# Kernel optimization log

Hardware: AMD Instinct MI355X
Metric: run time of the kernel (lower is better)

Reference implementation:

```python
import jax, jax.numpy as jnp
import numpy as np

B, T = 128, 64
N_IN, H1, H2, N_OUT = 2048, 2048, 1024, 128
BETA = 0.95
THRESH = 1.0  # snn.Leaky default threshold


def spike(x):
    # Heaviside firing function (forward of snntorch ATan surrogate)
    return (x > 0).astype(x.dtype)


def setup_inputs() -> dict:
    key = jax.random.key(0)
    ks = jax.random.split(key, 5)

    def linear_params(k, fan_in, fan_out):
        k1, k2 = jax.random.split(k)
        bound = 1.0 / np.sqrt(fan_in)  # torch nn.Linear default init
        W = jax.random.uniform(k1, (fan_out, fan_in), minval=-bound, maxval=bound, dtype=jnp.float32)
        b = jax.random.uniform(k2, (fan_out,), minval=-bound, maxval=bound, dtype=jnp.float32)
        return W, b

    W0, b0 = linear_params(ks[0], N_IN, N_IN)
    W1, b1 = linear_params(ks[1], N_IN, H1)
    W2, b2 = linear_params(ks[2], H1, H2)
    W3, b3 = linear_params(ks[3], H2, N_OUT)
    x = jax.random.normal(ks[4], (B, T, N_IN), dtype=jnp.float32)
    return {"x": x, "W0": W0, "b0": b0, "W1": W1, "b1": b1,
            "W2": W2, "b2": b2, "W3": W3, "b3": b3}


def _lif(cur, mem):
    # snntorch Leaky (reset_mechanism='subtract'): reset computed from incoming mem
    reset = spike(mem - THRESH)
    mem_new = BETA * mem + cur - reset * THRESH
    spk = spike(mem_new - THRESH)
    return spk, mem_new


def reference(x, W0, b0, W1, b1, W2, b2, W3, b3):
    Bb = x.shape[0]
    dt = x.dtype
    mems0 = (jnp.zeros((Bb, N_IN), dt), jnp.zeros((Bb, H1), dt),
             jnp.zeros((Bb, H2), dt), jnp.zeros((Bb, N_OUT), dt))
    x_tbf = jnp.swapaxes(x, 0, 1)  # [T, B, N_IN]

    def step(carry, x_t):
        m0, m1, m2, m3 = carry
        s0, m0 = _lif(x_t @ W0.T + b0, m0)
        s1, m1 = _lif(s0 @ W1.T + b1, m1)
        s2, m2 = _lif(s1 @ W2.T + b2, m2)
        s3, m3 = _lif(s2 @ W3.T + b3, m3)
        return (m0, m1, m2, m3), (s3, m3)

    _, (spk3, mem3) = jax.lax.scan(step, mems0, x_tbf)
    # [T, B, N_OUT] -> [B, T, N_OUT]
    return jnp.swapaxes(spk3, 0, 1), jnp.swapaxes(mem3, 0, 1)
```

## Files before the change

kernel.cpp:

```cpp
#include <hip/hip_runtime.h>
#include <cstddef>
#include <cstdint>


#define BETA 0.95f

static constexpr int B_ = 128;
static constexpr int T_ = 64;
static constexpr int M_ = B_ * T_;
static constexpr int NOUT = 128;

typedef __bf16 bf16x8 __attribute__((ext_vector_type(8)));
typedef _Float16 f16x8 __attribute__((ext_vector_type(8)));
typedef float f32x4 __attribute__((ext_vector_type(4)));
typedef ushort u16x8 __attribute__((ext_vector_type(8)));

__device__ __forceinline__ ushort f32_bf16_rne(float f) {
  uint32_t u = __float_as_uint(f);
  uint32_t r = u + 0x7FFFu + ((u >> 16) & 1u);
  return (ushort)(r >> 16);
}
__device__ __forceinline__ float bf16_f32(ushort h) {
  return __uint_as_float(((uint32_t)h) << 16);
}
__device__ __forceinline__ ushort h2u(_Float16 h) {
  union { _Float16 h; ushort u; } v; v.h = h; return v.u;
}
__device__ __forceinline__ _Float16 u2h(ushort u) {
  union { ushort u; _Float16 h; } v; v.u = u; return v.h;
}

__global__ __launch_bounds__(256) void split2_f16(
    const float* __restrict__ S, ushort* __restrict__ oh,
    ushort* __restrict__ ol, int K, int nslots)
{
  int g = blockIdx.x * 256 + threadIdx.x;
  if (g >= nslots) return;
  int spr = K >> 3;
  int row = g / spr;
  int sl = g - row * spr;
  int kb = sl >> 3;
  int slot = sl & 7;
  int pslot = (slot & 4) | ((slot & 3) ^ ((row >> 1) & 3));
  const float* src = S + (size_t)row * K + (kb << 6) + (slot << 3);
  size_t dst = (size_t)row * K + (kb << 6) + (pslot << 3);
  u16x8 vh, vl;
#pragma unroll
  for (int i = 0; i < 8; ++i) {
    float f = src[i];
    _Float16 h = (_Float16)f;
    float hf = (float)h;
    if (fabsf(hf) < 6.103515625e-05f) { h = (_Float16)0.0f; hf = 0.0f; }
    float l = (f - hf) * 4096.0f;
    _Float16 hl = (_Float16)l;
    vh[i] = h2u(h);
    vl[i] = h2u(hl);
  }
  *reinterpret_cast<u16x8*>(oh + dst) = vh;
  *reinterpret_cast<u16x8*>(ol + dst) = vl;
}

__global__ __launch_bounds__(256) void split3_swz(
    const float* __restrict__ S, ushort* __restrict__ o1,
    ushort* __restrict__ o2, ushort* __restrict__ o3,
    int K, int nslots)
{
  int g = blockIdx.x * 256 + threadIdx.x;
  if (g >= nslots) return;
  int spr = K >> 3;
  int row = g / spr;
  int sl = g - row * spr;
  int kb = sl >> 3;
  int slot = sl & 7;
  int pslot = slot ^ (row & 7);
  const float* src = S + (size_t)row * K + (kb << 6) + (slot << 3);
  size_t dst = (size_t)row * K + (kb << 6) + (pslot << 3);
  u16x8 v1, v2, v3;
#pragma unroll
  for (int i = 0; i < 8; ++i) {
    float f = src[i];
    ushort h1 = f32_bf16_rne(f);
    float r = f - bf16_f32(h1);
    ushort h2 = f32_bf16_rne(r);
    float r2 = r - bf16_f32(h2);
    ushort h3 = f32_bf16_rne(r2);
    v1[i] = h1; v2[i] = h2; v3[i] = h3;
  }
  *reinterpret_cast<u16x8*>(o1 + dst) = v1;
  *reinterpret_cast<u16x8*>(o2 + dst) = v2;
  *reinterpret_cast<u16x8*>(o3 + dst) = v3;
}

__global__ __launch_bounds__(256) void gemm_seg(
    const ushort* __restrict__ A0, const ushort* __restrict__ A1,
    const ushort* __restrict__ A2,
    const ushort* __restrict__ B0, const ushort* __restrict__ B1,
    const ushort* __restrict__ B2,
    int P, int apack, int bpack, int K, int N, int accum,
    float* __restrict__ C)
{
  __shared__ ushort As[128 * 64];
  __shared__ ushort Bs[128 * 64];

  const int tid = threadIdx.x;
  const int lane = tid & 63;
  const int wid = tid >> 6;
  const int wr = wid >> 1, wc = wid & 1;
  const int lane15 = lane & 15;
  const int lhi = lane >> 4;
  const int rswz = lane15 & 7;
  const int lrow = lane >> 3, lslot = lane & 7;

  int nwg = gridDim.x * gridDim.y;
  int bid = blockIdx.y * gridDim.x + blockIdx.x;
  int cpx = nwg >> 3;
  int sw = (bid & 7) * cpx + (bid >> 3);
  int bx = sw % gridDim.x, by = sw / gridDim.x;
  const int bm = by * 128, bn = bx * 128;

  f32x4 acc[4][4];
#pragma unroll
  for (int i = 0; i < 4; ++i)
#pragma unroll
    for (int j = 0; j < 4; ++j)
      acc[i][j] = (f32x4){0.f, 0.f, 0.f, 0.f};

  const bool isA = (wid < 2);
  ushort* lbase = isA ? As : Bs;
  const int rowbase0 = isA ? bm : bn;
  const int chunk0 = (wid & 1) * 8;

  for (int p = 0; p < P; ++p) {
    int ai = (apack >> (2 * p)) & 3;
    int bi = (bpack >> (2 * p)) & 3;
    const ushort* Ap = ai == 0 ? A0 : (ai == 1 ? A1 : A2);
    const ushort* Bp = bi == 0 ? B0 : (bi == 1 ? B1 : B2);
    const ushort* gsrc = isA ? Ap : Bp;
    for (int k0 = 0; k0 < K; k0 += 64) {
      __syncthreads();
#pragma unroll
      for (int c = 0; c < 8; ++c) {
        int chunk = chunk0 + c;
        int row = chunk * 8 + lrow;
        const ushort* g = gsrc + (size_t)(rowbase0 + row) * K + k0 + (lslot << 3);
        __builtin_amdgcn_global_load_lds(
            (const __attribute__((address_space(1))) void*)(g),
            (__attribute__((address_space(3))) void*)(lbase + chunk * 512),
            16, 0, 0);
      }
      __syncthreads();
#pragma unroll
      for (int kk = 0; kk < 2; ++kk) {
        int sp = ((kk << 2) | lhi) ^ rswz;
        bf16x8 af[4], bg[4];
#pragma unroll
        for (int i = 0; i < 4; ++i)
          af[i] = *(const bf16x8*)(As + (wr * 64 + i * 16 + lane15) * 64 + sp * 8);
#pragma unroll
        for (int j = 0; j < 4; ++j)
          bg[j] = *(const bf16x8*)(Bs + (wc * 64 + j * 16 + lane15) * 64 + sp * 8);
#pragma unroll
        for (int i = 0; i < 4; ++i)
#pragma unroll
          for (int j = 0; j < 4; ++j)
            acc[i][j] = __builtin_amdgcn_mfma_f32_16x16x32_bf16(
                af[i], bg[j], acc[i][j], 0, 0, 0);
      }
    }
  }

#pragma unroll
  for (int j = 0; j < 4; ++j) {
    int col = bn + wc * 64 + j * 16 + lane15;
#pragma unroll
    for (int i = 0; i < 4; ++i) {
      f32x4 v = acc[i][j];
      int r0 = bm + wr * 64 + i * 16 + lhi * 4;
      if (accum) {
#pragma unroll
        for (int r = 0; r < 4; ++r) {
          size_t idx = (size_t)(r0 + r) * N + col;
          C[idx] = C[idx] + v[r];
        }
      } else {
#pragma unroll
        for (int r = 0; r < 4; ++r)
          C[(size_t)(r0 + r) * N + col] = v[r];
      }
    }
  }
}

template<int NB, int MODE>
__global__ __launch_bounds__(512) void gemm2(
    const ushort* __restrict__ A,
    const ushort* __restrict__ Bs0, const ushort* __restrict__ Bs1,
    int NT, int K, int N,
    float* __restrict__ curM, ushort* __restrict__ curC)
{
  __shared__ __align__(16) ushort lds[32768 + 2 * 2 * NB * 4096];

  const int tid = threadIdx.x;
  const int lane = tid & 63;
  const int wid = tid >> 6;
  const int wm = wid >> 1;
  const int wn = wid & 1;
  const int lane15 = lane & 15;
  const int lhi = lane >> 4;
  const int sg2 = lhi ^ ((lane15 >> 1) & 3);

  int nwg = gridDim.x * gridDim.y;
  int bid = blockIdx.y * gridDim.x + blockIdx.x;
  int cpx = nwg >> 3;
  int sw = (bid & 7) * cpx + (bid >> 3);
  int bx = sw % gridDim.x, by = sw / gridDim.x;
  const int bm = by * 256, bn = bx * 128;

  const int sr2 = tid >> 2;
  const int sg = tid & 3;

  auto stage = [&](int t1, int h, int d) {
    const int k0 = t1 * 64 + h * 32;
#pragma unroll
    for (int l = 0; l < 2; ++l) {
      int row = sr2 + l * 128;
      __builtin_amdgcn_global_load_lds(
          (const __attribute__((address_space(1))) void*)(A + (size_t)(bm + row) * K + k0 + sg * 8),
          (__attribute__((address_space(3))) void*)(lds + d * 16384 + h * 8192 + row * 32 + sg * 8),
          16, 0, 0);
    }
#pragma unroll
    for (int s = 0; s < NB; ++s) {
      const ushort* Bp = (s == 0) ? Bs0 : Bs1;
      __builtin_amdgcn_global_load_lds(
          (const __attribute__((address_space(1))) void*)(Bp + (size_t)(bn + sr2) * K + k0 + sg * 8),
          (__attribute__((address_space(3))) void*)(lds + 32768 + ((d * 2 + h) * NB + s) * 4096 + sr2 * 32 + sg * 8),
          16, 0, 0);
    }
  };

  f32x4 accM[4][4], accC[4][4];
#pragma unroll
  for (int i = 0; i < 4; ++i)
#pragma unroll
    for (int j = 0; j < 4; ++j) {
      accM[i][j] = (f32x4){0.f, 0.f, 0.f, 0.f};
      accC[i][j] = (f32x4){0.f, 0.f, 0.f, 0.f};
    }

  stage(0, 0, 0);
  stage(0, 1, 0);
  if constexpr (NB == 2) asm volatile("s_waitcnt vmcnt(4)" ::: "memory");
  if constexpr (NB == 1) asm volatile("s_waitcnt vmcnt(3)" ::: "memory");
  asm volatile("s_barrier" ::: "memory");

  for (int t = 0; t < NT; ++t) {
    const int d = t & 1;
#pragma unroll
    for (int h = 0; h < 2; ++h) {
      f16x8 af[4];
      const ushort* Ab = lds + (d * 2 + h) * 8192;
#pragma unroll
      for (int i = 0; i < 4; ++i)
        af[i] = *(const f16x8*)(Ab + (wm * 64 + i * 16 + lane15) * 32 + sg2 * 8);

      if (t < NT - 1) {
        stage(t + 1, h, d ^ 1);
        if constexpr (NB == 2) asm volatile("s_waitcnt vmcnt(4)" ::: "memory");
        if constexpr (NB == 1) asm volatile("s_waitcnt vmcnt(3)" ::: "memory");
      } else if (h == 0) {
        asm volatile("s_waitcnt vmcnt(0)" ::: "memory");
      }
      asm volatile("s_barrier" ::: "memory");

      __builtin_amdgcn_s_setprio(1);
#pragma unroll
      for (int s = 0; s < NB; ++s) {
        const ushort* Bb = lds + 32768 + ((d * 2 + h) * NB + s) * 4096;
        f16x8 bf[4];
#pragma unroll
        for (int j = 0; j < 4; ++j)
          bf[j] = *(const f16x8*)(Bb + (wn * 64 + j * 16 + lane15) * 32 + sg2 * 8);
        if (MODE == 0 && s == 0) {
#pragma unroll
          for (int i = 0; i < 4; ++i)
#pragma unroll
            for (int j = 0; j < 4; ++j)
              accM[i][j] = __builtin_amdgcn_mfma_f32_16x16x32_f16(af[i], bf[j], accM[i][j], 0, 0, 0);
        } else {
#pragma unroll
          for (int i = 0; i < 4; ++i)
#pragma unroll
            for (int j = 0; j < 4; ++j)
              accC[i][j] = __builtin_amdgcn_mfma_f32_16x16x32_f16(af[i], bf[j], accC[i][j], 0, 0, 0);
        }
      }
      __builtin_amdgcn_s_setprio(0);
      asm volatile("s_barrier" ::: "memory");
    }
  }

#pragma unroll
  for (int i = 0; i < 4; ++i) {
    int r0 = bm + wm * 64 + i * 16 + lhi * 4;
#pragma unroll
    for (int j = 0; j < 4; ++j) {
      int col = bn + wn * 64 + j * 16 + lane15;
      f32x4 vc = accC[i][j];
      if (MODE == 0) {
        f32x4 vm = accM[i][j];
#pragma unroll
        for (int r = 0; r < 4; ++r) {
          size_t idx = (size_t)(r0 + r) * N + col;
          curM[idx] = vm[r];
          curC[idx] = h2u((_Float16)vc[r]);
        }
      } else {
#pragma unroll
        for (int r = 0; r < 4; ++r) {
          size_t idx = (size_t)(r0 + r) * N + col;
          float old = (float)u2h(curC[idx]);
          curC[idx] = h2u((_Float16)(old + vc[r]));
        }
      }
    }
  }
}

__global__ __launch_bounds__(256) void lif_comb(
    const float* __restrict__ curM, const ushort* __restrict__ curC,
    const float* __restrict__ bias, ushort* __restrict__ spk,
    int N, int total, int fmt)
{
  int g = blockIdx.x * 256 + threadIdx.x;
  if (g >= total) return;
  int b = g / N, n = g - b * N;
  int nb = n >> 6;
  int slot = (n >> 3) & 7;
  int nlow = n & 7;
  float bv = bias[n];
  const ushort one = fmt ? (ushort)0x3C00 : (ushort)0x3F80;
  float mem = 0.f;
  for (int t = 0; t < T_; ++t) {
    int m = b * T_ + t;
    size_t idx = (size_t)m * N + n;
    float mm = __fmaf_rn((float)u2h(curC[idx]), 2.44140625e-4f, curM[idx]);
    float c = __fadd_rn(mm, bv);
    float reset = ((mem - 1.0f) > 0.0f) ? 1.0f : 0.0f;
    mem = __fmul_rn(BETA, mem);
    mem = __fadd_rn(mem, c);
    mem = __fadd_rn(mem, -reset);
    ushort sv = ((mem - 1.0f) > 0.0f) ? one : (ushort)0;
    int ps = fmt ? ((slot & 4) | ((slot & 3) ^ ((m >> 1) & 3)))
                 : (slot ^ (m & 7));
    spk[(size_t)m * N + (nb << 6) + (ps << 3) + nlow] = sv;
  }
}

__global__ __launch_bounds__(256) void lif_final(
    const float* __restrict__ cur_in, const float* __restrict__ bias,
    float* __restrict__ spk_out, float* __restrict__ mem_out, int N, int total)
{
  int g = blockIdx.x * 256 + threadIdx.x;
  if (g >= total) return;
  int b = g / N, n = g - b * N;
  size_t base = (size_t)b * T_ * N + n;
  float bv = bias[n];
  float mem = 0.f;
  for (int t = 0; t < T_; ++t) {
    size_t idx = base + (size_t)t * N;
    float c = __fadd_rn(cur_in[idx], bv);
    float reset = ((mem - 1.0f) > 0.0f) ? 1.0f : 0.0f;
    mem = __fmul_rn(BETA, mem);
    mem = __fadd_rn(mem, c);
    mem = __fadd_rn(mem, -reset);
    spk_out[idx] = ((mem - 1.0f) > 0.0f) ? 1.0f : 0.0f;
    mem_out[idx] = mem;
  }
}

extern "C" void kernel_launch(void* const* d_in, const int* in_sizes, int n_in,
                              void* d_out, int out_size, void* d_ws, size_t ws_size,
                              hipStream_t stream)
{
  const float* x  = (const float*)d_in[0];
  const float* W0 = (const float*)d_in[1];
  const float* b0 = (const float*)d_in[2];
  const float* W1 = (const float*)d_in[3];
  const float* b1 = (const float*)d_in[4];
  const float* W2 = (const float*)d_in[5];
  const float* b2 = (const float*)d_in[6];
  const float* W3 = (const float*)d_in[7];
  const float* b3 = (const float*)d_in[8];
  float* out = (float*)d_out;

  char* ws = (char*)d_ws;
  size_t off = 0;
  auto take = [&](size_t bytes) -> char* {
    char* p = ws + off;
    off += (bytes + 255) & ~(size_t)255;
    return p;
  };

  ushort* w0h = (ushort*)take((size_t)2048 * 2048 * 2);
  ushort* w0l = (ushort*)take((size_t)2048 * 2048 * 2);
  ushort* w1h = (ushort*)take((size_t)2048 * 2048 * 2);
  ushort* w1l = (ushort*)take((size_t)2048 * 2048 * 2);
  ushort* w2h = (ushort*)take((size_t)1024 * 2048 * 2);
  ushort* w2l = (ushort*)take((size_t)1024 * 2048 * 2);
  ushort* w3s[3];
  for (int i = 0; i < 3; ++i) w3s[i] = (ushort*)take((size_t)128 * 1024 * 2);
  ushort* xh = (ushort*)take((size_t)M_ * 2048 * 2);
  ushort* xl = (ushort*)take((size_t)M_ * 2048 * 2);
  ushort* s0 = (ushort*)take((size_t)M_ * 2048 * 2);
  float* curM = (float*)take((size_t)M_ * 2048 * 4);
  ushort* curC = (ushort*)take((size_t)M_ * 2048 * 2);
  ushort* s1 = xh;
  ushort* s2 = xl;

  dim3 blk(256);
  dim3 fblk(512);

  {
    int ns = 2048 * 2048 / 8;
    split2_f16<<<(ns + 255) / 256, blk, 0, stream>>>(W0, w0h, w0l, 2048, ns);
    split2_f16<<<(ns + 255) / 256, blk, 0, stream>>>(W1, w1h, w1l, 2048, ns);
    ns = 1024 * 2048 / 8;
    split2_f16<<<(ns + 255) / 256, blk, 0, stream>>>(W2, w2h, w2l, 2048, ns);
    ns = 128 * 1024 / 8;
    split3_swz<<<(ns + 255) / 256, blk, 0, stream>>>(W3, w3s[0], w3s[1], w3s[2], 1024, ns);
    ns = M_ * 2048 / 8;
    split2_f16<<<(ns + 255) / 256, blk, 0, stream>>>(x, xh, xl, 2048, ns);
  }

  {
    dim3 grid(2048 / 128, M_ / 256);
    gemm2<2, 0><<<grid, fblk, 0, stream>>>(xh, w0h, w0l, 32, 2048, 2048, curM, curC);
    gemm2<1, 1><<<grid, fblk, 0, stream>>>(xl, w0h, w0h, 32, 2048, 2048, curM, curC);
    lif_comb<<<(B_ * 2048) / 256, blk, 0, stream>>>(curM, curC, b0, s0, 2048, B_ * 2048, 1);
  }
  {
    dim3 grid(2048 / 128, M_ / 256);
    gemm2<2, 0><<<grid, fblk, 0, stream>>>(s0, w1h, w1l, 32, 2048, 2048, curM, curC);
    lif_comb<<<(B_ * 2048) / 256, blk, 0, stream>>>(curM, curC, b1, s1, 2048, B_ * 2048, 1);
  }
  {
    dim3 grid(1024 / 128, M_ / 256);
    gemm2<2, 0><<<grid, fblk, 0, stream>>>(s1, w2h, w2l, 32, 2048, 1024, curM, curC);
    lif_comb<<<(B_ * 1024) / 256, blk, 0, stream>>>(curM, curC, b2, s2, 1024, B_ * 1024, 0);
  }
  {
    dim3 grid(128 / 128, M_ / 128);
    gemm_seg<<<grid, blk, 0, stream>>>(s2, s2, s2, w3s[0], w3s[1], w3s[2],
                                       1, 0, 0, 1024, 128, 0, curM);
    gemm_seg<<<grid, blk, 0, stream>>>(s2, s2, s2, w3s[0], w3s[1], w3s[2],
                                       2, 0, 1 | (2 << 2), 1024, 128, 1, curM);
    float* spk3 = out;
    float* mem3 = out + (size_t)M_ * NOUT;
    lif_final<<<(B_ * NOUT) / 256, blk, 0, stream>>>(curM, b3, spk3, mem3, NOUT, B_ * NOUT);
  }
}
```

Measured before the change: 591.6 us.

## Fuse LIF recurrence into GEMM epilogues and drop fp32 current buffer

```diff
diff --git a/kernel.cpp b/kernel.cpp
--- a/kernel.cpp
+++ b/kernel.cpp
@@ -52,9 +52,8 @@
     float hf = (float)h;
     if (fabsf(hf) < 6.103515625e-05f) { h = (_Float16)0.0f; hf = 0.0f; }
     float l = (f - hf) * 4096.0f;
-    _Float16 hl = (_Float16)l;
     vh[i] = h2u(h);
-    vl[i] = h2u(hl);
+    vl[i] = h2u((_Float16)l);
   }
   *reinterpret_cast<u16x8*>(oh + dst) = vh;
   *reinterpret_cast<u16x8*>(ol + dst) = vl;
@@ -91,16 +90,269 @@
   *reinterpret_cast<u16x8*>(o3 + dst) = v3;
 }
 
-__global__ __launch_bounds__(256) void gemm_seg(
-    const ushort* __restrict__ A0, const ushort* __restrict__ A1,
-    const ushort* __restrict__ A2,
+__global__ __launch_bounds__(512) void gemm_corr(
+    const ushort* __restrict__ A, const ushort* __restrict__ Bh,
+    int NT, int K, int N, ushort* __restrict__ curC)
+{
+  __shared__ __align__(16) ushort lds[49152];
+
+  const int tid = threadIdx.x;
+  const int lane = tid & 63;
+  const int wid = tid >> 6;
+  const int wm = wid >> 1;
+  const int wn = wid & 1;
+  const int lane15 = lane & 15;
+  const int lhi = lane >> 4;
+  const int sg2 = lhi ^ ((lane15 >> 1) & 3);
+
+  int nwg = gridDim.x * gridDim.y;
+  int bid = blockIdx.y * gridDim.x + blockIdx.x;
+  int cpx = nwg >> 3;
+  int sw = (bid & 7) * cpx + (bid >> 3);
+  int bx = sw % gridDim.x, by = sw / gridDim.x;
+  const int bm = by * 256, bn = bx * 128;
+
+  const int sr2 = tid >> 2;
+  const int sg = tid & 3;
+
+  auto stage = [&](int t1, int h, int d) {
+    const int k0 = t1 * 64 + h * 32;
+#pragma unroll
+    for (int l = 0; l < 2; ++l) {
+      int row = sr2 + l * 128;
+      __builtin_amdgcn_global_load_lds(
+          (const __attribute__((address_space(1))) void*)(A + (size_t)(bm + row) * K + k0 + sg * 8),
+          (__attribute__((address_space(3))) void*)(lds + d * 16384 + h * 8192 + row * 32 + sg * 8),
+          16, 0, 0);
+    }
+    __builtin_amdgcn_global_load_lds(
+        (const __attribute__((address_space(1))) void*)(Bh + (size_t)(bn + sr2) * K + k0 + sg * 8),
+        (__attribute__((address_space(3))) void*)(lds + 32768 + (d * 2 + h) * 4096 + sr2 * 32 + sg * 8),
+        16, 0, 0);
+  };
+
+  f32x4 accC[4][4];
+#pragma unroll
+  for (int i = 0; i < 4; ++i)
+#pragma unroll
+    for (int j = 0; j < 4; ++j)
+      accC[i][j] = (f32x4){0.f, 0.f, 0.f, 0.f};
+
+  stage(0, 0, 0);
+  stage(0, 1, 0);
+  asm volatile("s_waitcnt vmcnt(3)" ::: "memory");
+  asm volatile("s_barrier" ::: "memory");
+
+  for (int t = 0; t < NT; ++t) {
+    const int d = t & 1;
+#pragma unroll
+    for (int h = 0; h < 2; ++h) {
+      f16x8 af[4];
+      const ushort* Ab = lds + (d * 2 + h) * 8192;
+#pragma unroll
+      for (int i = 0; i < 4; ++i)
+        af[i] = *(const f16x8*)(Ab + (wm * 64 + i * 16 + lane15) * 32 + sg2 * 8);
+
+      if (t < NT - 1) {
+        stage(t + 1, h, d ^ 1);
+        asm volatile("s_waitcnt vmcnt(3)" ::: "memory");
+      } else if (h == 0) {
+        asm volatile("s_waitcnt vmcnt(0)" ::: "memory");
+      }
+      asm volatile("s_barrier" ::: "memory");
+
+      const ushort* Bb = lds + 32768 + (d * 2 + h) * 4096;
+      f16x8 bf[4];
+#pragma unroll
+      for (int j = 0; j < 4; ++j)
+        bf[j] = *(const f16x8*)(Bb + (wn * 64 + j * 16 + lane15) * 32 + sg2 * 8);
+      __builtin_amdgcn_s_setprio(1);
+#pragma unroll
+      for (int i = 0; i < 4; ++i)
+#pragma unroll
+        for (int j = 0; j < 4; ++j)
+          accC[i][j] = __builtin_amdgcn_mfma_f32_16x16x32_f16(af[i], bf[j], accC[i][j], 0, 0, 0);
+      __builtin_amdgcn_s_setprio(0);
+      asm volatile("s_barrier" ::: "memory");
+    }
+  }
+
+#pragma unroll
+  for (int i = 0; i < 4; ++i) {
+    int r0 = bm + wm * 64 + i * 16 + lhi * 4;
+#pragma unroll
+    for (int j = 0; j < 4; ++j) {
+      int col = bn + wn * 64 + j * 16 + lane15;
+      f32x4 vc = accC[i][j];
+#pragma unroll
+      for (int r = 0; r < 4; ++r)
+        curC[(size_t)(r0 + r) * N + col] = h2u((_Float16)vc[r]);
+    }
+  }
+}
+
+template<int HASC, int FMT>
+__global__ __launch_bounds__(512) void gemm_mainL(
+    const ushort* __restrict__ A,
+    const ushort* __restrict__ Bh, const ushort* __restrict__ Bl,
+    int NT, int K, int N,
+    const ushort* __restrict__ curCin,
+    const float* __restrict__ bias, ushort* __restrict__ spk)
+{
+  __shared__ __align__(16) ushort lds[67584];
+
+  const int tid = threadIdx.x;
+  const int lane = tid & 63;
+  const int wid = tid >> 6;
+  const int wm = wid >> 1;
+  const int wn = wid & 1;
+  const int lane15 = lane & 15;
+  const int lhi = lane >> 4;
+  const int sg2 = lhi ^ ((lane15 >> 1) & 3);
+
+  int nwg = gridDim.x * gridDim.y;
+  int bid = blockIdx.y * gridDim.x + blockIdx.x;
+  int cpx = nwg >> 3;
+  int sw = (bid & 7) * cpx + (bid >> 3);
+  int bx = sw % gridDim.x, by = sw / gridDim.x;
+  const int bm = by * 256, bn = bx * 128;
+
+  const int sr2 = tid >> 2;
+  const int sg = tid & 3;
+
+  auto stage = [&](int t1, int h, int d) {
+    const int k0 = t1 * 64 + h * 32;
+#pragma unroll
+    for (int l = 0; l < 2; ++l) {
+      int row = sr2 + l * 128;
+      __builtin_amdgcn_global_load_lds(
+          (const __attribute__((address_space(1))) void*)(A + (size_t)(bm + row) * K + k0 + sg * 8),
+          (__attribute__((address_space(3))) void*)(lds + d * 16384 + h * 8192 + row * 32 + sg * 8),
+          16, 0, 0);
+    }
+#pragma unroll
+    for (int s = 0; s < 2; ++s) {
+      const ushort* Bp = (s == 0) ? Bh : Bl;
+      __builtin_amdgcn_global_load_lds(
+          (const __attribute__((address_space(1))) void*)(Bp + (size_t)(bn + sr2) * K + k0 + sg * 8),
+          (__attribute__((address_space(3))) void*)(lds + 32768 + ((d * 2 + h) * 2 + s) * 4096 + sr2 * 32 + sg * 8),
+          16, 0, 0);
+    }
+  };
+
+  f32x4 accM[4][4], accC[4][4];
+#pragma unroll
+  for (int i = 0; i < 4; ++i)
+#pragma unroll
+    for (int j = 0; j < 4; ++j) {
+      accM[i][j] = (f32x4){0.f, 0.f, 0.f, 0.f};
+      accC[i][j] = (f32x4){0.f, 0.f, 0.f, 0.f};
+    }
+
+  stage(0, 0, 0);
+  stage(0, 1, 0);
+  asm volatile("s_waitcnt vmcnt(4)" ::: "memory");
+  asm volatile("s_barrier" ::: "memory");
+
+  for (int t = 0; t < NT; ++t) {
+    const int d = t & 1;
+#pragma unroll
+    for (int h = 0; h < 2; ++h) {
+      f16x8 af[4];
+      const ushort* Ab = lds + (d * 2 + h) * 8192;
+#pragma unroll
+      for (int i = 0; i < 4; ++i)
+        af[i] = *(const f16x8*)(Ab + (wm * 64 + i * 16 + lane15) * 32 + sg2 * 8);
+
+      if (t < NT - 1) {
+        stage(t + 1, h, d ^ 1);
+        asm volatile("s_waitcnt vmcnt(4)" ::: "memory");
+      } else if (h == 0) {
+        asm volatile("s_waitcnt vmcnt(0)" ::: "memory");
+      }
+      asm volatile("s_barrier" ::: "memory");
+
+      __builtin_amdgcn_s_setprio(1);
+#pragma unroll
+      for (int s = 0; s < 2; ++s) {
+        const ushort* Bb = lds + 32768 + ((d * 2 + h) * 2 + s) * 4096;
+        f16x8 bf[4];
+#pragma unroll
+        for (int j = 0; j < 4; ++j)
+          bf[j] = *(const f16x8*)(Bb + (wn * 64 + j * 16 + lane15) * 32 + sg2 * 8);
+        if (s == 0) {
+#pragma unroll
+          for (int i = 0; i < 4; ++i)
+#pragma unroll
+            for (int j = 0; j < 4; ++j)
+              accM[i][j] = __builtin_amdgcn_mfma_f32_16x16x32_f16(af[i], bf[j], accM[i][j], 0, 0, 0);
+        } else {
+#pragma unroll
+          for (int i = 0; i < 4; ++i)
+#pragma unroll
+            for (int j = 0; j < 4; ++j)
+              accC[i][j] = __builtin_amdgcn_mfma_f32_16x16x32_f16(af[i], bf[j], accC[i][j], 0, 0, 0);
+        }
+      }
+      __builtin_amdgcn_s_setprio(0);
+      asm volatile("s_barrier" ::: "memory");
+    }
+  }
+
+  float* curb = (float*)lds;
+#pragma unroll
+  for (int i = 0; i < 4; ++i) {
+    int rl = wm * 64 + i * 16 + lhi * 4;
+#pragma unroll
+    for (int j = 0; j < 4; ++j) {
+      int cl = wn * 64 + j * 16 + lane15;
+      f32x4 vm = accM[i][j], vc = accC[i][j];
+#pragma unroll
+      for (int r = 0; r < 4; ++r) {
+        float corr = vc[r];
+        if (HASC)
+          corr += (float)u2h(curCin[(size_t)(bm + rl + r) * N + (bn + cl)]);
+        curb[(rl + r) * 132 + cl] = __fmaf_rn(corr, 2.44140625e-4f, vm[r]);
+      }
+    }
+  }
+  __syncthreads();
+
+  {
+    int b2 = tid >> 7;
+    int n = tid & 127;
+    int cg = bn + n;
+    float bv = bias[cg];
+    int nb6 = cg >> 6;
+    int sl = (cg >> 3) & 7;
+    int nlow = cg & 7;
+    const ushort one = FMT ? (ushort)0x3C00 : (ushort)0x3F80;
+    float mem = 0.f;
+    for (int t2 = 0; t2 < 64; ++t2) {
+      float c = __fadd_rn(curb[(b2 * 64 + t2) * 132 + n], bv);
+      float reset = ((mem - 1.0f) > 0.0f) ? 1.0f : 0.0f;
+      mem = __fmul_rn(BETA, mem);
+      mem = __fadd_rn(mem, c);
+      mem = __fadd_rn(mem, -reset);
+      ushort sv = ((mem - 1.0f) > 0.0f) ? one : (ushort)0;
+      int m = bm + b2 * 64 + t2;
+      int ps = FMT ? ((sl & 4) | ((sl & 3) ^ ((m >> 1) & 3)))
+                   : (sl ^ (m & 7));
+      spk[(size_t)m * N + (nb6 << 6) + (ps << 3) + nlow] = sv;
+    }
+  }
+}
+
+__global__ __launch_bounds__(256) void gemm_seg_lif(
+    const ushort* __restrict__ A0,
     const ushort* __restrict__ B0, const ushort* __restrict__ B1,
     const ushort* __restrict__ B2,
-    int P, int apack, int bpack, int K, int N, int accum,
-    float* __restrict__ C)
+    const float* __restrict__ bias,
+    float* __restrict__ spk_out, float* __restrict__ mem_out)
 {
   __shared__ ushort As[128 * 64];
   __shared__ ushort Bs[128 * 64];
+  __shared__ float curb[128 * 132];
 
   const int tid = threadIdx.x;
   const int lane = tid & 63;
@@ -118,31 +370,30 @@
   int bx = sw % gridDim.x, by = sw / gridDim.x;
   const int bm = by * 128, bn = bx * 128;
 
-  f32x4 acc[4][4];
+  f32x4 accM[4][4], accC[4][4];
 #pragma unroll
   for (int i = 0; i < 4; ++i)
 #pragma unroll
-    for (int j = 0; j < 4; ++j)
-      acc[i][j] = (f32x4){0.f, 0.f, 0.f, 0.f};
+    for (int j = 0; j < 4; ++j) {
+      accM[i][j] = (f32x4){0.f, 0.f, 0.f, 0.f};
+      accC[i][j] = (f32x4){0.f, 0.f, 0.f, 0.f};
+    }
 
   const bool isA = (wid < 2);
   ushort* lbase = isA ? As : Bs;
   const int rowbase0 = isA ? bm : bn;
   const int chunk0 = (wid & 1) * 8;
 
-  for (int p = 0; p < P; ++p) {
-    int ai = (apack >> (2 * p)) & 3;
-    int bi = (bpack >> (2 * p)) & 3;
-    const ushort* Ap = ai == 0 ? A0 : (ai == 1 ? A1 : A2);
-    const ushort* Bp = bi == 0 ? B0 : (bi == 1 ? B1 : B2);
-    const ushort* gsrc = isA ? Ap : Bp;
-    for (int k0 = 0; k0 < K; k0 += 64) {
+  for (int p = 0; p < 3; ++p) {
+    const ushort* Bp = (p == 0) ? B0 : ((p == 1) ? B1 : B2);
+    const ushort* gsrc = isA ? A0 : Bp;
+    for (int k0 = 0; k0 < 1024; k0 += 64) {
       __syncthreads();
 #pragma unroll
       for (int c = 0; c < 8; ++c) {
         int chunk = chunk0 + c;
         int row = chunk * 8 + lrow;
-        const ushort* g = gsrc + (size_t)(rowbase0 + row) * K + k0 + (lslot << 3);
+        const ushort* g = gsrc + (size_t)(rowbase0 + row) * 1024 + k0 + (lslot << 3);
         __builtin_amdgcn_global_load_lds(
             (const __attribute__((address_space(1))) void*)(g),
             (__attribute__((address_space(3))) void*)(lbase + chunk * 512),
@@ -159,223 +410,54 @@
 #pragma unroll
         for (int j = 0; j < 4; ++j)
           bg[j] = *(const bf16x8*)(Bs + (wc * 64 + j * 16 + lane15) * 64 + sp * 8);
-#pragma unroll
-        for (int i = 0; i < 4; ++i)
-#pragma unroll
-          for (int j = 0; j < 4; ++j)
-            acc[i][j] = __builtin_amdgcn_mfma_f32_16x16x32_bf16(
-                af[i], bg[j], acc[i][j], 0, 0, 0);
-      }
-    }
-  }
-
-#pragma unroll
-  for (int j = 0; j < 4; ++j) {
-    int col = bn + wc * 64 + j * 16 + lane15;
-#pragma unroll
-    for (int i = 0; i < 4; ++i) {
-      f32x4 v = acc[i][j];
-      int r0 = bm + wr * 64 + i * 16 + lhi * 4;
-      if (accum) {
-#pragma unroll
-        for (int r = 0; r < 4; ++r) {
-          size_t idx = (size_t)(r0 + r) * N + col;
-          C[idx] = C[idx] + v[r];
-        }
-      } else {
-#pragma unroll
-        for (int r = 0; r < 4; ++r)
-          C[(size_t)(r0 + r) * N + col] = v[r];
-      }
-    }
-  }
-}
-
-template<int NB, int MODE>
-__global__ __launch_bounds__(512) void gemm2(
-    const ushort* __restrict__ A,
-    const ushort* __restrict__ Bs0, const ushort* __restrict__ Bs1,
-    int NT, int K, int N,
-    float* __restrict__ curM, ushort* __restrict__ curC)
-{
-  __shared__ __align__(16) ushort lds[32768 + 2 * 2 * NB * 4096];
-
-  const int tid = threadIdx.x;
-  const int lane = tid & 63;
-  const int wid = tid >> 6;
-  const int wm = wid >> 1;
-  const int wn = wid & 1;
-  const int lane15 = lane & 15;
-  const int lhi = lane >> 4;
-  const int sg2 = lhi ^ ((lane15 >> 1) & 3);
-
-  int nwg = gridDim.x * gridDim.y;
-  int bid = blockIdx.y * gridDim.x + blockIdx.x;
-  int cpx = nwg >> 3;
-  int sw = (bid & 7) * cpx + (bid >> 3);
-  int bx = sw % gridDim.x, by = sw / gridDim.x;
-  const int bm = by * 256, bn = bx * 128;
-
-  const int sr2 = tid >> 2;
-  const int sg = tid & 3;
-
-  auto stage = [&](int t1, int h, int d) {
-    const int k0 = t1 * 64 + h * 32;
-#pragma unroll
-    for (int l = 0; l < 2; ++l) {
-      int row = sr2 + l * 128;
-      __builtin_amdgcn_global_load_lds(
-          (const __attribute__((address_space(1))) void*)(A + (size_t)(bm + row) * K + k0 + sg * 8),
-          (__attribute__((address_space(3))) void*)(lds + d * 16384 + h * 8192 + row * 32 + sg * 8),
-          16, 0, 0);
-    }
-#pragma unroll
-    for (int s = 0; s < NB; ++s) {
-      const ushort* Bp = (s == 0) ? Bs0 : Bs1;
-      __builtin_amdgcn_global_load_lds(
-          (const __attribute__((address_space(1))) void*)(Bp + (size_t)(bn + sr2) * K + k0 + sg * 8),
-          (__attribute__((address_space(3))) void*)(lds + 32768 + ((d * 2 + h) * NB + s) * 4096 + sr2 * 32 + sg * 8),
-          16, 0, 0);
-    }
-  };
-
-  f32x4 accM[4][4], accC[4][4];
-#pragma unroll
-  for (int i = 0; i < 4; ++i)
-#pragma unroll
-    for (int j = 0; j < 4; ++j) {
-      accM[i][j] = (f32x4){0.f, 0.f, 0.f, 0.f};
-      accC[i][j] = (f32x4){0.f, 0.f, 0.f, 0.f};
-    }
-
-  stage(0, 0, 0);
-  stage(0, 1, 0);
-  if constexpr (NB == 2) asm volatile("s_waitcnt vmcnt(4)" ::: "memory");
-  if constexpr (NB == 1) asm volatile("s_waitcnt vmcnt(3)" ::: "memory");
-  asm volatile("s_barrier" ::: "memory");
-
-  for (int t = 0; t < NT; ++t) {
-    const int d = t & 1;
-#pragma unroll
-    for (int h = 0; h < 2; ++h) {
-      f16x8 af[4];
-      const ushort* Ab = lds + (d * 2 + h) * 8192;
-#pragma unroll
-      for (int i = 0; i < 4; ++i)
-        af[i] = *(const f16x8*)(Ab + (wm * 64 + i * 16 + lane15) * 32 + sg2 * 8);
-
-      if (t < NT - 1) {
-        stage(t + 1, h, d ^ 1);
-        if constexpr (NB == 2) asm volatile("s_waitcnt vmcnt(4)" ::: "memory");
-        if constexpr (NB == 1) asm volatile("s_waitcnt vmcnt(3)" ::: "memory");
-      } else if (h == 0) {
-        asm volatile("s_waitcnt vmcnt(0)" ::: "memory");
-      }
-      asm volatile("s_barrier" ::: "memory");
-
-      __builtin_amdgcn_s_setprio(1);
-#pragma unroll
-      for (int s = 0; s < NB; ++s) {
-        const ushort* Bb = lds + 32768 + ((d * 2 + h) * NB + s) * 4096;
-        f16x8 bf[4];
-#pragma unroll
-        for (int j = 0; j < 4; ++j)
-          bf[j] = *(const f16x8*)(Bb + (wn * 64 + j * 16 + lane15) * 32 + sg2 * 8);
-        if (MODE == 0 && s == 0) {
+        if (p == 0) {
 #pragma unroll
           for (int i = 0; i < 4; ++i)
 #pragma unroll
             for (int j = 0; j < 4; ++j)
-              accM[i][j] = __builtin_amdgcn_mfma_f32_16x16x32_f16(af[i], bf[j], accM[i][j], 0, 0, 0);
+              accM[i][j] = __builtin_amdgcn_mfma_f32_16x16x32_bf16(af[i], bg[j], accM[i][j], 0, 0, 0);
         } else {
 #pragma unroll
           for (int i = 0; i < 4; ++i)
 #pragma unroll
             for (int j = 0; j < 4; ++j)
-              accC[i][j] = __builtin_amdgcn_mfma_f32_16x16x32_f16(af[i], bf[j], accC[i][j], 0, 0, 0);
+              accC[i][j] = __builtin_amdgcn_mfma_f32_16x16x32_bf16(af[i], bg[j], accC[i][j], 0, 0, 0);
         }
       }
-      __builtin_amdgcn_s_setprio(0);
-      asm volatile("s_barrier" ::: "memory");
-    }
-  }
-
-#pragma unroll
-  for (int i = 0; i < 4; ++i) {
-    int r0 = bm + wm * 64 + i * 16 + lhi * 4;
-#pragma unroll
-    for (int j = 0; j < 4; ++j) {
-      int col = bn + wn * 64 + j * 16 + lane15;
-      f32x4 vc = accC[i][j];
-      if (MODE == 0) {
-        f32x4 vm = accM[i][j];
-#pragma unroll
-        for (int r = 0; r < 4; ++r) {
-          size_t idx = (size_t)(r0 + r) * N + col;
-          curM[idx] = vm[r];
-          curC[idx] = h2u((_Float16)vc[r]);
-        }
-      } else {
-#pragma unroll
-        for (int r = 0; r < 4; ++r) {
-          size_t idx = (size_t)(r0 + r) * N + col;
-          float old = (float)u2h(curC[idx]);
-          curC[idx] = h2u((_Float16)(old + vc[r]));
-        }
-      }
-    }
-  }
-}
-
-__global__ __launch_bounds__(256) void lif_comb(
-    const float* __restrict__ curM, const ushort* __restrict__ curC,
-    const float* __restrict__ bias, ushort* __restrict__ spk,
-    int N, int total, int fmt)
-{
-  int g = blockIdx.x * 256 + threadIdx.x;
-  if (g >= total) return;
-  int b = g / N, n = g - b * N;
-  int nb = n >> 6;
-  int slot = (n >> 3) & 7;
-  int nlow = n & 7;
-  float bv = bias[n];
-  const ushort one = fmt ? (ushort)0x3C00 : (ushort)0x3F80;
-  float mem = 0.f;
-  for (int t = 0; t < T_; ++t) {
-    int m = b * T_ + t;
-    size_t idx = (size_t)m * N + n;
-    float mm = __fmaf_rn((float)u2h(curC[idx]), 2.44140625e-4f, curM[idx]);
-    float c = __fadd_rn(mm, bv);
-    float reset = ((mem - 1.0f) > 0.0f) ? 1.0f : 0.0f;
-    mem = __fmul_rn(BETA, mem);
-    mem = __fadd_rn(mem, c);
-    mem = __fadd_rn(mem, -reset);
-    ushort sv = ((mem - 1.0f) > 0.0f) ? one : (ushort)0;
-    int ps = fmt ? ((slot & 4) | ((slot & 3) ^ ((m >> 1) & 3)))
-                 : (slot ^ (m & 7));
-    spk[(size_t)m * N + (nb << 6) + (ps << 3) + nlow] = sv;
-  }
-}
-
-__global__ __launch_bounds__(256) void lif_final(
-    const float* __restrict__ cur_in, const float* __restrict__ bias,
-    float* __restrict__ spk_out, float* __restrict__ mem_out, int N, int total)
-{
-  int g = blockIdx.x * 256 + threadIdx.x;
-  if (g >= total) return;
-  int b = g / N, n = g - b * N;
-  size_t base = (size_t)b * T_ * N + n;
-  float bv = bias[n];
-  float mem = 0.f;
-  for (int t = 0; t < T_; ++t) {
-    size_t idx = base + (size_t)t * N;
-    float c = __fadd_rn(cur_in[idx], bv);
-    float reset = ((mem - 1.0f) > 0.0f) ? 1.0f : 0.0f;
-    mem = __fmul_rn(BETA, mem);
-    mem = __fadd_rn(mem, c);
-    mem = __fadd_rn(mem, -reset);
-    spk_out[idx] = ((mem - 1.0f) > 0.0f) ? 1.0f : 0.0f;
-    mem_out[idx] = mem;
+    }
+  }
+
+  __syncthreads();
+#pragma unroll
+  for (int j = 0; j < 4; ++j) {
+    int cl = wc * 64 + j * 16 + lane15;
+#pragma unroll
+    for (int i = 0; i < 4; ++i) {
+      int rl = wr * 64 + i * 16 + lhi * 4;
+      f32x4 vm = accM[i][j], vc = accC[i][j];
+#pragma unroll
+      for (int r = 0; r < 4; ++r)
+        curb[(rl + r) * 132 + cl] = vm[r] + vc[r];
+    }
+  }
+  __syncthreads();
+
+  {
+    int b2 = tid >> 7;
+    int n = tid & 127;
+    float bv = bias[bn + n];
+    float mem = 0.f;
+    for (int t2 = 0; t2 < 64; ++t2) {
+      float c = __fadd_rn(curb[(b2 * 64 + t2) * 132 + n], bv);
+      float reset = ((mem - 1.0f) > 0.0f) ? 1.0f : 0.0f;
+      mem = __fmul_rn(BETA, mem);
+      mem = __fadd_rn(mem, c);
+      mem = __fadd_rn(mem, -reset);
+      int m = bm + b2 * 64 + t2;
+      size_t idx = (size_t)m * 128 + bn + n;
+      spk_out[idx] = ((mem - 1.0f) > 0.0f) ? 1.0f : 0.0f;
+      mem_out[idx] = mem;
+    }
   }
 }
 
@@ -413,7 +495,6 @@
   ushort* xh = (ushort*)take((size_t)M_ * 2048 * 2);
   ushort* xl = (ushort*)take((size_t)M_ * 2048 * 2);
   ushort* s0 = (ushort*)take((size_t)M_ * 2048 * 2);
-  float* curM = (float*)take((size_t)M_ * 2048 * 4);
   ushort* curC = (ushort*)take((size_t)M_ * 2048 * 2);
   ushort* s1 = xh;
   ushort* s2 = xl;
@@ -435,28 +516,20 @@
 
   {
     dim3 grid(2048 / 128, M_ / 256);
-    gemm2<2, 0><<<grid, fblk, 0, stream>>>(xh, w0h, w0l, 32, 2048, 2048, curM, curC);
-    gemm2<1, 1><<<grid, fblk, 0, stream>>>(xl, w0h, w0h, 32, 2048, 2048, curM, curC);
-    lif_comb<<<(B_ * 2048) / 256, blk, 0, stream>>>(curM, curC, b0, s0, 2048, B_ * 2048, 1);
+    gemm_corr<<<grid, fblk, 0, stream>>>(xl, w0h, 32, 2048, 2048, curC);
+    gemm_mainL<1, 1><<<grid, fblk, 0, stream>>>(xh, w0h, w0l, 32, 2048, 2048, curC, b0, s0);
   }
   {
     dim3 grid(2048 / 128, M_ / 256);
-    gemm2<2, 0><<<grid, fblk, 0, stream>>>(s0, w1h, w1l, 32, 2048, 2048, curM, curC);
-    lif_comb<<<(B_ * 2048) / 256, blk, 0, stream>>>(curM, curC, b1, s1, 2048, B_ * 2048, 1);
+    gemm_mainL<0, 1><<<grid, fblk, 0, stream>>>(s0, w1h, w1l, 32, 2048, 2048, nullptr, b1, s1);
   }
   {
     dim3 grid(1024 / 128, M_ / 256);
-    gemm2<2, 0><<<grid, fblk, 0, stream>>>(s1, w2h, w2l, 32, 2048, 1024, curM, curC);
-    lif_comb<<<(B_ * 1024) / 256, blk, 0, stream>>>(curM, curC, b2, s2, 1024, B_ * 1024, 0);
-  }
-  {
-    dim3 grid(128 / 128, M_ / 128);
-    gemm_seg<<<grid, blk, 0, stream>>>(s2, s2, s2, w3s[0], w3s[1], w3s[2],
-                                       1, 0, 0, 1024, 128, 0, curM);
-    gemm_seg<<<grid, blk, 0, stream>>>(s2, s2, s2, w3s[0], w3s[1], w3s[2],
-                                       2, 0, 1 | (2 << 2), 1024, 128, 1, curM);
+    gemm_mainL<0, 0><<<grid, fblk, 0, stream>>>(s1, w2h, w2l, 32, 2048, 1024, nullptr, b2, s2);
+  }
+  {
     float* spk3 = out;
     float* mem3 = out + (size_t)M_ * NOUT;
-    lif_final<<<(B_ * NOUT) / 256, blk, 0, stream>>>(curM, b3, spk3, mem3, NOUT, B_ * NOUT);
-  }
-}
+    gemm_seg_lif<<<dim3(1, 64), blk, 0, stream>>>(s2, w3s[0], w3s[1], w3s[2], b3, spk3, mem3);
+  }
+}
```

Result: faster. 478.8 us (-19.1%).
